# Performance work log

Measured on AMD Instinct MI355X. Metric: run time of the kernel, lower is better.

## Reference

```python
import jax, jax.numpy as jnp
import numpy as np

N_NODES = 10000
N_EDGES = 80000
F_IN = 128
H1 = 2048
H2 = 2048
H3 = 1024


def _sgconv(x, pos, src, dst, W_in, b_in, W_out, b_out):
    # geo-GCN SpatialGraphConv with hidden_size=1:
    # message(j->i) = relu(Linear(pos_j - pos_i)) * x_j ; aggr='add' ; then Linear out
    rel = pos[src] - pos[dst]                      # [E, 2]  (pos_j - pos_i)
    scale = jax.nn.relu(rel @ W_in + b_in)         # [E, C_in]
    msg = scale * x[src]                           # [E, C_in]
    agg = jax.ops.segment_sum(msg, dst, num_segments=x.shape[0])  # [N, C_in]
    return agg @ W_out + b_out                     # [N, C_out]


def setup_inputs() -> dict:
    key = jax.random.key(0)
    ks = jax.random.split(key, 12)
    x = jax.random.normal(ks[0], (N_NODES, F_IN), dtype=jnp.float32)
    pos = jax.random.normal(ks[1], (N_NODES, 2), dtype=jnp.float32)
    edge_index = jax.random.randint(ks[2], (2, N_EDGES), 0, N_NODES, dtype=jnp.int32)

    def lin(k, fan_in, fan_out):
        lim = 1.0 / np.sqrt(fan_in)
        kw, kb = jax.random.split(k)
        W = jax.random.uniform(kw, (fan_in, fan_out), jnp.float32, -lim, lim)
        b = jax.random.uniform(kb, (fan_out,), jnp.float32, -lim, lim)
        return W, b

    W_in1, b_in1 = lin(ks[3], 2, F_IN)
    W_out1, b_out1 = lin(ks[4], F_IN, H1)
    W_in2, b_in2 = lin(ks[5], 2, H1)
    W_out2, b_out2 = lin(ks[6], H1, H2)
    W_in3, b_in3 = lin(ks[7], 2, H2)
    W_out3, b_out3 = lin(ks[8], H2, H3)

    return {
        "x": x, "pos": pos, "edge_index": edge_index,
        "W_in1": W_in1, "b_in1": b_in1, "W_out1": W_out1, "b_out1": b_out1,
        "W_in2": W_in2, "b_in2": b_in2, "W_out2": W_out2, "b_out2": b_out2,
        "W_in3": W_in3, "b_in3": b_in3, "W_out3": W_out3, "b_out3": b_out3,
    }


def reference(x, pos, edge_index,
              W_in1, b_in1, W_out1, b_out1,
              W_in2, b_in2, W_out2, b_out2,
              W_in3, b_in3, W_out3, b_out3):
    src, dst = edge_index[0], edge_index[1]  # flow source_to_target: j=src, i=dst
    h = jax.nn.relu(_sgconv(x, pos, src, dst, W_in1, b_in1, W_out1, b_out1))
    h = jax.nn.relu(_sgconv(h, pos, src, dst, W_in2, b_in2, W_out2, b_out2))
    h = jax.nn.relu(_sgconv(h, pos, src, dst, W_in3, b_in3, W_out3, b_out3))
    # F.normalize(h, dim=1): L2 normalize rows with eps clamp 1e-12
    norm = jnp.linalg.norm(h, axis=1, keepdims=True)
    return h / jnp.maximum(norm, 1e-12)
```

## Files before the change

### kernel.cpp

```cpp
#include <hip/hip_runtime.h>
#include <hip/hip_bf16.h>

#define DEVI __device__ __forceinline__

constexpr int NN = 10000;
constexpr int NE = 80000;
constexpr int AGG_ROWS = 10240;
constexpr int ES_CAP = 110016;

typedef __attribute__((ext_vector_type(8))) short bf16x8;
typedef __attribute__((ext_vector_type(4))) float f32x4;

DEVI float blo(unsigned int u) {
  union { unsigned int i; float f; } c; c.i = u << 16; return c.f;
}
DEVI float bhi(unsigned int u) {
  union { unsigned int i; float f; } c; c.i = u & 0xffff0000u; return c.f;
}
DEVI unsigned short f2b(float f) {
  union { float f; unsigned int i; } c; c.f = f;
  unsigned int i = c.i;
  return (unsigned short)((i + 0x7fffu + ((i >> 16) & 1u)) >> 16);
}
DEVI void st1(float* p, float v) { *p = v; }
DEVI void st1(unsigned short* p, float v) { *p = f2b(v); }
DEVI void store8b(unsigned short* p, const float v[8]) {
  int4 pk;
  pk.x = (int)((unsigned)f2b(v[0]) | ((unsigned)f2b(v[1]) << 16));
  pk.y = (int)((unsigned)f2b(v[2]) | ((unsigned)f2b(v[3]) << 16));
  pk.z = (int)((unsigned)f2b(v[4]) | ((unsigned)f2b(v[5]) << 16));
  pk.w = (int)((unsigned)f2b(v[6]) | ((unsigned)f2b(v[7]) << 16));
  *reinterpret_cast<int4*>(p) = pk;
}

DEVI void gload16(const void* g, void* l) {
  __builtin_amdgcn_global_load_lds(
      (const __attribute__((address_space(1))) void*)g,
      (__attribute__((address_space(3))) void*)l, 16, 0, 0);
}

__global__ __launch_bounds__(256)
void hist_kernel(const int* __restrict__ dst, int* __restrict__ cnt) {
  int e = blockIdx.x * 256 + threadIdx.x;
  if (e < NE) atomicAdd(&cnt[dst[e]], 1);
}

__global__ __launch_bounds__(1024)
void scan_kernel(const int* __restrict__ cnt, int* __restrict__ off,
                 int* __restrict__ cursor) {
  __shared__ int wpart[16];
  __shared__ int carry;
  int tid = threadIdx.x, lane = tid & 63, w = tid >> 6;
  if (tid == 0) carry = 0;
  __syncthreads();
  for (int base = 0; base < NN; base += 1024) {
    int i = base + tid;
    int v = (i < NN) ? ((cnt[i] + 3) & ~3) : 0;
    int s = v;
#pragma unroll
    for (int o = 1; o < 64; o <<= 1) { int t = __shfl_up(s, o); if (lane >= o) s += t; }
    if (lane == 63) wpart[w] = s;
    __syncthreads();
    if (w == 0) {
      int ws = (lane < 16) ? wpart[lane] : 0;
#pragma unroll
      for (int o = 1; o < 16; o <<= 1) { int t = __shfl_up(ws, o); if (lane >= o) ws += t; }
      if (lane < 16) wpart[lane] = ws;
    }
    __syncthreads();
    int ex = carry + (w ? wpart[w - 1] : 0) + s - v;
    if (i < NN) { off[i] = ex; cursor[i] = ex; }
    __syncthreads();
    if (tid == 0) carry += wpart[15];
    __syncthreads();
  }
}

__global__ __launch_bounds__(256)
void bucket_kernel(const int* __restrict__ src, const int* __restrict__ dst,
                   const float* __restrict__ pos,
                   int* __restrict__ cursor, int* __restrict__ es,
                   float* __restrict__ rel) {
  int e = blockIdx.x * 256 + threadIdx.x;
  if (e < NE) {
    int s = src[e], d = dst[e];
    int p = atomicAdd(&cursor[d], 1);
    float2 ps = *reinterpret_cast<const float2*>(pos + 2 * s);
    float2 pd = *reinterpret_cast<const float2*>(pos + 2 * d);
    es[p] = s;
    *reinterpret_cast<float2*>(rel + 2 * p) = make_float2(ps.x - pd.x, ps.y - pd.y);
  }
}

__global__ __launch_bounds__(256)
void transpose_w(const float* __restrict__ W, unsigned short* __restrict__ WT,
                 int K, int N) {
  __shared__ float tile[32][33];
  int tx = threadIdx.x & 31, ty = threadIdx.x >> 5;
  int n0 = blockIdx.x * 32, k0 = blockIdx.y * 32;
#pragma unroll
  for (int j = 0; j < 32; j += 8)
    tile[ty + j][tx] = W[(size_t)(k0 + ty + j) * N + n0 + tx];
  __syncthreads();
#pragma unroll
  for (int j = 0; j < 32; j += 8)
    WT[(size_t)(n0 + ty + j) * K + k0 + tx] = f2b(tile[tx][ty + j]);
}

__global__ __launch_bounds__(256)
void gather_l1(const float* __restrict__ x,
               const int* __restrict__ off, const int* __restrict__ cnt,
               const int* __restrict__ es, const float* __restrict__ rel,
               const float* __restrict__ Win, const float* __restrict__ bin,
               unsigned short* __restrict__ agg) {
  constexpr int C = 128;
  int lane = threadIdx.x & 63;
  int i = blockIdx.x * 4 + (threadIdx.x >> 6);
  if (i >= NN) return;
  int c = lane * 2;
  float w00 = Win[c], w01 = Win[c + 1];
  float w10 = Win[C + c], w11 = Win[C + c + 1];
  float b0 = bin[c], b1 = bin[c + 1];
  float a0 = 0.f, a1 = 0.f;
  int s0 = off[i], n = cnt[i];

  for (int k = 0; k < n; k += 4) {
    int4 s4 = *reinterpret_cast<const int4*>(es + s0 + k);
    float4 ra = *reinterpret_cast<const float4*>(rel + 2 * (s0 + k));
    float4 rb = *reinterpret_cast<const float4*>(rel + 2 * (s0 + k) + 4);
    float2 q0 = *reinterpret_cast<const float2*>(x + (size_t)s4.x * C + c);
    float2 q1 = *reinterpret_cast<const float2*>(x + (size_t)s4.y * C + c);
    float2 q2 = *reinterpret_cast<const float2*>(x + (size_t)s4.z * C + c);
    float2 q3 = *reinterpret_cast<const float2*>(x + (size_t)s4.w * C + c);
    {
      float sc0 = fmaxf(fmaf(ra.x, w00, fmaf(ra.y, w10, b0)), 0.f);
      float sc1 = fmaxf(fmaf(ra.x, w01, fmaf(ra.y, w11, b1)), 0.f);
      a0 = fmaf(sc0, q0.x, a0); a1 = fmaf(sc1, q0.y, a1);
    }
    if (k + 1 < n) {
      float sc0 = fmaxf(fmaf(ra.z, w00, fmaf(ra.w, w10, b0)), 0.f);
      float sc1 = fmaxf(fmaf(ra.z, w01, fmaf(ra.w, w11, b1)), 0.f);
      a0 = fmaf(sc0, q1.x, a0); a1 = fmaf(sc1, q1.y, a1);
    }
    if (k + 2 < n) {
      float sc0 = fmaxf(fmaf(rb.x, w00, fmaf(rb.y, w10, b0)), 0.f);
      float sc1 = fmaxf(fmaf(rb.x, w01, fmaf(rb.y, w11, b1)), 0.f);
      a0 = fmaf(sc0, q2.x, a0); a1 = fmaf(sc1, q2.y, a1);
    }
    if (k + 3 < n) {
      float sc0 = fmaxf(fmaf(rb.z, w00, fmaf(rb.w, w10, b0)), 0.f);
      float sc1 = fmaxf(fmaf(rb.z, w01, fmaf(rb.w, w11, b1)), 0.f);
      a0 = fmaf(sc0, q3.x, a0); a1 = fmaf(sc1, q3.y, a1);
    }
  }
  unsigned int pk = (unsigned)f2b(a0) | ((unsigned)f2b(a1) << 16);
  *reinterpret_cast<unsigned int*>(agg + (size_t)i * C + c) = pk;
}

__global__ __launch_bounds__(256)
void gather_chunk(const unsigned short* __restrict__ x,
                  const int* __restrict__ off, const int* __restrict__ cnt,
                  const int* __restrict__ es, const float* __restrict__ rel,
                  const float* __restrict__ Win, const float* __restrict__ bin,
                  unsigned short* __restrict__ agg, int ngb8) {
  constexpr int C = 2048;
  constexpr int V = 8;
  int wgid = blockIdx.x;
  int half = wgid >= ngb8;
  int base = half ? wgid - ngb8 : wgid;
  int chunk = (base & 7) + (half << 3);
  int grp = base >> 3;
  int lane = threadIdx.x & 63;
  int wid = threadIdx.x >> 6;
  int slot = lane >> 4;
  int l16 = lane & 15;
  int i = grp * 16 + wid * 4 + slot;
  int c = chunk * 128 + l16 * V;

  float w0[V], w1[V], bb[V], acc[V];
#pragma unroll
  for (int j = 0; j < V; ++j) {
    w0[j] = Win[c + j]; w1[j] = Win[C + c + j]; bb[j] = bin[c + j]; acc[j] = 0.f;
  }
  int s0 = off[i], n = cnt[i];

  auto fma8 = [&](float rx, float ry, const int4& q) {
    float xv[V] = { blo(q.x), bhi(q.x), blo(q.y), bhi(q.y),
                    blo(q.z), bhi(q.z), blo(q.w), bhi(q.w) };
#pragma unroll
    for (int j = 0; j < V; ++j) {
      float sc = fmaxf(fmaf(rx, w0[j], fmaf(ry, w1[j], bb[j])), 0.f);
      acc[j] = fmaf(sc, xv[j], acc[j]);
    }
  };
  for (int k = 0; k < n; k += 4) {
    int4 s4 = *reinterpret_cast<const int4*>(es + s0 + k);
    float4 ra = *reinterpret_cast<const float4*>(rel + 2 * (s0 + k));
    float4 rb = *reinterpret_cast<const float4*>(rel + 2 * (s0 + k) + 4);
    int4 q0 = *reinterpret_cast<const int4*>(x + (size_t)s4.x * C + c);
    int4 q1 = *reinterpret_cast<const int4*>(x + (size_t)s4.y * C + c);
    int4 q2 = *reinterpret_cast<const int4*>(x + (size_t)s4.z * C + c);
    int4 q3 = *reinterpret_cast<const int4*>(x + (size_t)s4.w * C + c);
    fma8(ra.x, ra.y, q0);
    if (k + 1 < n) fma8(ra.z, ra.w, q1);
    if (k + 2 < n) fma8(rb.x, rb.y, q2);
    if (k + 3 < n) fma8(rb.z, rb.w, q3);
  }
  store8b(agg + (size_t)i * C + c, acc);
}

template <typename OT>
__global__ __launch_bounds__(256, 2)
void gemm320(const unsigned short* __restrict__ A,
             const unsigned short* __restrict__ BT,
             const float* __restrict__ bias, OT* __restrict__ out,
             int M, int N, int K) {
  __shared__ unsigned short lds[2 * 14336];
  const int t = threadIdx.x;
  const int lane = t & 63, wid = t >> 6;
  const int wr = wid >> 1, wc = wid & 1;

  const int nwg = gridDim.x * gridDim.y;
  const int orig = blockIdx.y * gridDim.x + blockIdx.x;
  const int swz = (orig & 7) * (nwg >> 3) + (orig >> 3);
  const int bx = swz % gridDim.x, by = swz / gridDim.x;
  const int m0 = by * 320, n0 = bx * 128;
  const int nk = K >> 5;

  const unsigned short* gA = A + (size_t)(m0 + lane) * K + wid * 8;
  const unsigned short* gB = BT + (size_t)(n0 + lane) * K + wid * 8;
  const int lA0 = wid * 2560 + lane * 8;
  const int lB0 = 10240 + wid * 1024 + lane * 8;

  auto STAGE = [&](int buf, int kt) {
    const unsigned short* ga = gA + kt * 32;
    const unsigned short* gb = gB + kt * 32;
    unsigned short* la = lds + buf * 14336 + lA0;
    unsigned short* lb = lds + buf * 14336 + lB0;
#pragma unroll
    for (int jj = 0; jj < 5; ++jj)
      gload16(ga + (size_t)(jj * 64) * K, la + jj * 512);
#pragma unroll
    for (int jj = 0; jj < 2; ++jj)
      gload16(gb + (size_t)(jj * 64) * K, lb + jj * 512);
  };

  const int frow = lane & 15, fch = lane >> 4;
  const int paOff = fch * 2560 + (wr * 160 + frow) * 8;
  const int pbOff = 10240 + fch * 1024 + (wc * 64 + frow) * 8;

  f32x4 acc[10][4];
#pragma unroll
  for (int m = 0; m < 10; ++m)
#pragma unroll
    for (int n = 0; n < 4; ++n) acc[m][n] = 0.f;

  STAGE(0, 0);

  int cur = 0;
  for (int kt = 0; kt < nk; ++kt) {
    if (kt + 1 < nk) {
      STAGE(cur ^ 1, kt + 1);
      asm volatile("s_waitcnt vmcnt(7)" ::: "memory");
    } else {
      asm volatile("s_waitcnt vmcnt(0)" ::: "memory");
    }
    asm volatile("s_barrier" ::: "memory");
    const unsigned short* pa = lds + cur * 14336 + paOff;
    const unsigned short* pb = lds + cur * 14336 + pbOff;
    bf16x8 bf[4];
#pragma unroll
    for (int n = 0; n < 4; ++n)
      bf[n] = *reinterpret_cast<const bf16x8*>(pb + n * 128);
    __builtin_amdgcn_s_setprio(1);
#pragma unroll
    for (int m = 0; m < 10; ++m) {
      bf16x8 af = *reinterpret_cast<const bf16x8*>(pa + m * 128);
#pragma unroll
      for (int n = 0; n < 4; ++n)
        acc[m][n] = __builtin_amdgcn_mfma_f32_16x16x32_bf16(
            af, bf[n], acc[m][n], 0, 0, 0);
    }
    __builtin_amdgcn_s_setprio(0);
    asm volatile("s_barrier" ::: "memory");
    cur ^= 1;
  }

  const int ccol = lane & 15;
  const int crow = (lane >> 4) * 4;
  float bv[4];
#pragma unroll
  for (int n = 0; n < 4; ++n)
    bv[n] = bias[n0 + wc * 64 + n * 16 + ccol];
#pragma unroll
  for (int m = 0; m < 10; ++m) {
    int gm0 = m0 + wr * 160 + m * 16 + crow;
#pragma unroll
    for (int r = 0; r < 4; ++r) {
      int gm = gm0 + r;
      if (gm < M) {
        size_t base = (size_t)gm * N + n0 + wc * 64 + ccol;
#pragma unroll
        for (int n = 0; n < 4; ++n)
          st1(out + base + n * 16, fmaxf(acc[m][n][r] + bv[n], 0.f));
      }
    }
  }
}

__global__ __launch_bounds__(256)
void l2norm_kernel(float* __restrict__ out) {
  constexpr int C = 1024;
  float* p = out + (size_t)blockIdx.x * C;
  float4 v = *reinterpret_cast<const float4*>(p + threadIdx.x * 4);
  float s = v.x * v.x + v.y * v.y + v.z * v.z + v.w * v.w;
#pragma unroll
  for (int o = 32; o > 0; o >>= 1) s += __shfl_down(s, o);
  __shared__ float wsum[4];
  if ((threadIdx.x & 63) == 0) wsum[threadIdx.x >> 6] = s;
  __syncthreads();
  float tot = wsum[0] + wsum[1] + wsum[2] + wsum[3];
  float inv = 1.0f / fmaxf(sqrtf(tot), 1e-12f);
  float4 r = make_float4(v.x * inv, v.y * inv, v.z * inv, v.w * inv);
  *reinterpret_cast<float4*>(p + threadIdx.x * 4) = r;
}

extern "C" void kernel_launch(void* const* d_in, const int* in_sizes, int n_in,
                              void* d_out, int out_size, void* d_ws, size_t ws_size,
                              hipStream_t stream) {
  (void)in_sizes; (void)n_in; (void)out_size; (void)ws_size;
  const float* x     = (const float*)d_in[0];
  const float* pos   = (const float*)d_in[1];
  const int*   ei    = (const int*)d_in[2];
  const int*   srcv  = ei;
  const int*   dstv  = ei + NE;
  const float* Win1  = (const float*)d_in[3];
  const float* bin1  = (const float*)d_in[4];
  const float* Wout1 = (const float*)d_in[5];
  const float* bout1 = (const float*)d_in[6];
  const float* Win2  = (const float*)d_in[7];
  const float* bin2  = (const float*)d_in[8];
  const float* Wout2 = (const float*)d_in[9];
  const float* bout2 = (const float*)d_in[10];
  const float* Win3  = (const float*)d_in[11];
  const float* bin3  = (const float*)d_in[12];
  const float* Wout3 = (const float*)d_in[13];
  const float* bout3 = (const float*)d_in[14];
  float* outp = (float*)d_out;

  char* ws = (char*)d_ws;
  unsigned short* aggb = (unsigned short*)ws;
  unsigned short* h1   = (unsigned short*)(ws + 41943040);
  unsigned short* W2T  = (unsigned short*)(ws + 82903040);
  unsigned short* W3T  = (unsigned short*)(ws + 91291648);
  unsigned short* W1T  = (unsigned short*)(ws + 95485952);
  int* cnt    = (int*)(ws + 96010240);
  int* off    = (int*)(ws + 96050240);
  int* cursor = (int*)(ws + 96090240);
  int* es     = (int*)(ws + 96130240);
  float* rel  = (float*)(ws + 96570304);
  unsigned short* h2 = (unsigned short*)d_out;

  const dim3 blk(256);
  const int eb = (NE + 255) / 256;
  const int ngb8 = ((NN + 15) / 16) * 8;

  hipMemsetAsync(cnt, 0, NN * sizeof(int), stream);
  hipMemsetAsync(es, 0, ES_CAP * sizeof(int), stream);
  hist_kernel<<<eb, blk, 0, stream>>>(dstv, cnt);
  scan_kernel<<<1, 1024, 0, stream>>>(cnt, off, cursor);
  bucket_kernel<<<eb, blk, 0, stream>>>(srcv, dstv, pos, cursor, es, rel);

  transpose_w<<<dim3(2048 / 32, 128 / 32),  blk, 0, stream>>>(Wout1, W1T, 128, 2048);
  transpose_w<<<dim3(2048 / 32, 2048 / 32), blk, 0, stream>>>(Wout2, W2T, 2048, 2048);
  transpose_w<<<dim3(1024 / 32, 2048 / 32), blk, 0, stream>>>(Wout3, W3T, 2048, 1024);

  hipMemsetAsync(aggb + (size_t)NN * 2048, 0, (size_t)(AGG_ROWS - NN) * 2048 * 2, stream);

  gather_l1<<<(NN + 3) / 4, blk, 0, stream>>>(x, off, cnt, es, rel, Win1, bin1, aggb);
  gemm320<unsigned short><<<dim3(2048 / 128, AGG_ROWS / 320), blk, 0, stream>>>(
      aggb, W1T, bout1, h1, NN, 2048, 128);

  gather_chunk<<<2 * ngb8, blk, 0, stream>>>(h1, off, cnt, es, rel, Win2, bin2, aggb, ngb8);
  gemm320<unsigned short><<<dim3(2048 / 128, AGG_ROWS / 320), blk, 0, stream>>>(
      aggb, W2T, bout2, h2, NN, 2048, 2048);

  gather_chunk<<<2 * ngb8, blk, 0, stream>>>(h2, off, cnt, es, rel, Win3, bin3, aggb, ngb8);
  gemm320<float><<<dim3(1024 / 128, AGG_ROWS / 320), blk, 0, stream>>>(
      aggb, W3T, bout3, outp, NN, 1024, 2048);

  l2norm_kernel<<<NN, blk, 0, stream>>>(outp);
}
```

Measured before the change: 371.0 us.

## Rewrite GEMM as 8-wave 320x256 tile with BK=64 and XOR-swizzled LDS

Replaces the 4-wave 320x128 GEMM with an 8-wave kernel computing a 320x256 tile and a K step of 64. It uses 144KB of dynamic LDS with XOR-swizzled row chunks to avoid bank conflicts. The MFMA loop is split into four ping-pong phases separated by barriers. The aim is more reuse per LDS load and better overlap of loads with MFMA work, at the cost of heavy LDS use (one block per CU), fewer blocks per GEMM, and more barriers.

```diff
diff --git a/kernel.cpp b/kernel.cpp
--- a/kernel.cpp
+++ b/kernel.cpp
@@ -210,44 +210,44 @@
 }
 
 template <typename OT>
-__global__ __launch_bounds__(256, 2)
-void gemm320(const unsigned short* __restrict__ A,
-             const unsigned short* __restrict__ BT,
-             const float* __restrict__ bias, OT* __restrict__ out,
-             int M, int N, int K) {
-  __shared__ unsigned short lds[2 * 14336];
+__global__ __launch_bounds__(512, 2)
+void gemm8p(const unsigned short* __restrict__ A,
+            const unsigned short* __restrict__ BT,
+            const float* __restrict__ bias, OT* __restrict__ out,
+            int M, int N, int K) {
+  extern __shared__ unsigned short lds[];
   const int t = threadIdx.x;
   const int lane = t & 63, wid = t >> 6;
-  const int wr = wid >> 1, wc = wid & 1;
+  const int wr = wid >> 2, wc = wid & 3;
 
   const int nwg = gridDim.x * gridDim.y;
   const int orig = blockIdx.y * gridDim.x + blockIdx.x;
   const int swz = (orig & 7) * (nwg >> 3) + (orig >> 3);
   const int bx = swz % gridDim.x, by = swz / gridDim.x;
-  const int m0 = by * 320, n0 = bx * 128;
-  const int nk = K >> 5;
-
-  const unsigned short* gA = A + (size_t)(m0 + lane) * K + wid * 8;
-  const unsigned short* gB = BT + (size_t)(n0 + lane) * K + wid * 8;
-  const int lA0 = wid * 2560 + lane * 8;
-  const int lB0 = 10240 + wid * 1024 + lane * 8;
+  const int m0 = by * 320, n0 = bx * 256;
+  const int nk = K >> 6;
+
+  const int srow = t >> 3;
+  const int schunk = (t & 7) ^ (srow & 7);
+  const unsigned short* gA = A + (size_t)(m0 + srow) * K + schunk * 8;
+  const unsigned short* gB = BT + (size_t)(n0 + srow) * K + schunk * 8;
+  const int lt8 = t * 8;
 
   auto STAGE = [&](int buf, int kt) {
-    const unsigned short* ga = gA + kt * 32;
-    const unsigned short* gb = gB + kt * 32;
-    unsigned short* la = lds + buf * 14336 + lA0;
-    unsigned short* lb = lds + buf * 14336 + lB0;
+    const size_t ko = (size_t)kt << 6;
+    unsigned short* lb = lds + buf * 36864;
 #pragma unroll
     for (int jj = 0; jj < 5; ++jj)
-      gload16(ga + (size_t)(jj * 64) * K, la + jj * 512);
-#pragma unroll
-    for (int jj = 0; jj < 2; ++jj)
-      gload16(gb + (size_t)(jj * 64) * K, lb + jj * 512);
+      gload16(gA + (size_t)(jj * 64) * K + ko, lb + jj * 4096 + lt8);
+#pragma unroll
+    for (int jj = 0; jj < 4; ++jj)
+      gload16(gB + (size_t)(jj * 64) * K + ko, lb + 20480 + jj * 4096 + lt8);
   };
 
-  const int frow = lane & 15, fch = lane >> 4;
-  const int paOff = fch * 2560 + (wr * 160 + frow) * 8;
-  const int pbOff = 10240 + fch * 1024 + (wc * 64 + frow) * 8;
+  const int frow = lane & 15, kc = lane >> 4;
+  const int sl0 = (kc ^ (frow & 7)) * 8;
+  const int paRow = (wr * 160 + frow) * 64;
+  const int pbRow = 20480 + (wc * 64 + frow) * 64;
 
   f32x4 acc[10][4];
 #pragma unroll
@@ -261,28 +261,76 @@
   for (int kt = 0; kt < nk; ++kt) {
     if (kt + 1 < nk) {
       STAGE(cur ^ 1, kt + 1);
-      asm volatile("s_waitcnt vmcnt(7)" ::: "memory");
+      asm volatile("s_waitcnt vmcnt(9)" ::: "memory");
     } else {
       asm volatile("s_waitcnt vmcnt(0)" ::: "memory");
     }
-    asm volatile("s_barrier" ::: "memory");
-    const unsigned short* pa = lds + cur * 14336 + paOff;
-    const unsigned short* pb = lds + cur * 14336 + pbOff;
-    bf16x8 bf[4];
+    __builtin_amdgcn_s_barrier();
+    const unsigned short* pa = lds + cur * 36864 + paRow;
+    const unsigned short* pb = lds + cur * 36864 + pbRow;
+    bf16x8 bf[4], af[5];
+
 #pragma unroll
     for (int n = 0; n < 4; ++n)
-      bf[n] = *reinterpret_cast<const bf16x8*>(pb + n * 128);
+      bf[n] = *reinterpret_cast<const bf16x8*>(pb + n * 1024 + sl0);
+#pragma unroll
+    for (int m = 0; m < 5; ++m)
+      af[m] = *reinterpret_cast<const bf16x8*>(pa + m * 1024 + sl0);
+    __builtin_amdgcn_s_barrier();
     __builtin_amdgcn_s_setprio(1);
 #pragma unroll
-    for (int m = 0; m < 10; ++m) {
-      bf16x8 af = *reinterpret_cast<const bf16x8*>(pa + m * 128);
+    for (int m = 0; m < 5; ++m)
 #pragma unroll
       for (int n = 0; n < 4; ++n)
         acc[m][n] = __builtin_amdgcn_mfma_f32_16x16x32_bf16(
-            af, bf[n], acc[m][n], 0, 0, 0);
-    }
+            af[m], bf[n], acc[m][n], 0, 0, 0);
     __builtin_amdgcn_s_setprio(0);
-    asm volatile("s_barrier" ::: "memory");
+    __builtin_amdgcn_s_barrier();
+
+#pragma unroll
+    for (int m = 0; m < 5; ++m)
+      af[m] = *reinterpret_cast<const bf16x8*>(pa + (5 + m) * 1024 + sl0);
+    __builtin_amdgcn_s_barrier();
+    __builtin_amdgcn_s_setprio(1);
+#pragma unroll
+    for (int m = 0; m < 5; ++m)
+#pragma unroll
+      for (int n = 0; n < 4; ++n)
+        acc[5 + m][n] = __builtin_amdgcn_mfma_f32_16x16x32_bf16(
+            af[m], bf[n], acc[5 + m][n], 0, 0, 0);
+    __builtin_amdgcn_s_setprio(0);
+    __builtin_amdgcn_s_barrier();
+
+#pragma unroll
+    for (int n = 0; n < 4; ++n)
+      bf[n] = *reinterpret_cast<const bf16x8*>(pb + n * 1024 + (sl0 ^ 32));
+#pragma unroll
+    for (int m = 0; m < 5; ++m)
+      af[m] = *reinterpret_cast<const bf16x8*>(pa + m * 1024 + (sl0 ^ 32));
+    __builtin_amdgcn_s_barrier();
+    __builtin_amdgcn_s_setprio(1);
+#pragma unroll
+    for (int m = 0; m < 5; ++m)
+#pragma unroll
+      for (int n = 0; n < 4; ++n)
+        acc[m][n] = __builtin_amdgcn_mfma_f32_16x16x32_bf16(
+            af[m], bf[n], acc[m][n], 0, 0, 0);
+    __builtin_amdgcn_s_setprio(0);
+    __builtin_amdgcn_s_barrier();
+
+#pragma unroll
+    for (int m = 0; m < 5; ++m)
+      af[m] = *reinterpret_cast<const bf16x8*>(pa + (5 + m) * 1024 + (sl0 ^ 32));
+    __builtin_amdgcn_s_barrier();
+    __builtin_amdgcn_s_setprio(1);
+#pragma unroll
+    for (int m = 0; m < 5; ++m)
+#pragma unroll
+      for (int n = 0; n < 4; ++n)
+        acc[5 + m][n] = __builtin_amdgcn_mfma_f32_16x16x32_bf16(
+            af[m], bf[n], acc[5 + m][n], 0, 0, 0);
+    __builtin_amdgcn_s_setprio(0);
+    __builtin_amdgcn_s_barrier();
     cur ^= 1;
   }
 
@@ -361,6 +409,11 @@
   float* rel  = (float*)(ws + 96570304);
   unsigned short* h2 = (unsigned short*)d_out;
 
+  hipFuncSetAttribute((const void*)gemm8p<unsigned short>,
+                      hipFuncAttributeMaxDynamicSharedMemorySize, 147456);
+  hipFuncSetAttribute((const void*)gemm8p<float>,
+                      hipFuncAttributeMaxDynamicSharedMemorySize, 147456);
+
   const dim3 blk(256);
   const int eb = (NE + 255) / 256;
   const int ngb8 = ((NN + 15) / 16) * 8;
@@ -378,15 +431,15 @@
   hipMemsetAsync(aggb + (size_t)NN * 2048, 0, (size_t)(AGG_ROWS - NN) * 2048 * 2, stream);
 
   gather_l1<<<(NN + 3) / 4, blk, 0, stream>>>(x, off, cnt, es, rel, Win1, bin1, aggb);
-  gemm320<unsigned short><<<dim3(2048 / 128, AGG_ROWS / 320), blk, 0, stream>>>(
+  gemm8p<unsigned short><<<dim3(2048 / 256, AGG_ROWS / 320), 512, 147456, stream>>>(
       aggb, W1T, bout1, h1, NN, 2048, 128);
 
   gather_chunk<<<2 * ngb8, blk, 0, stream>>>(h1, off, cnt, es, rel, Win2, bin2, aggb, ngb8);
-  gemm320<unsigned short><<<dim3(2048 / 128, AGG_ROWS / 320), blk, 0, stream>>>(
+  gemm8p<unsigned short><<<dim3(2048 / 256, AGG_ROWS / 320), 512, 147456, stream>>>(
       aggb, W2T, bout2, h2, NN, 2048, 2048);
 
   gather_chunk<<<2 * ngb8, blk, 0, stream>>>(h2, off, cnt, es, rel, Win3, bin3, aggb, ngb8);
-  gemm320<float><<<dim3(1024 / 128, AGG_ROWS / 320), blk, 0, stream>>>(
+  gemm8p<float><<<dim3(1024 / 256, AGG_ROWS / 320), 512, 147456, stream>>>(
       aggb, W3T, bout3, outp, NN, 1024, 2048);
 
   l2norm_kernel<<<NN, blk, 0, stream>>>(outp);
```

After: 342.5 us. 7.7% less time.
